# Optimization experiments

Hardware: AMD Instinct MI355X
Metric: run time of the kernel (lower is better)

Reference implementation:

```python
import jax, jax.numpy as jnp
import numpy as np

B, S, H = 8, 1024, 1024
NH, HD = 16, 64
MBANK, TOPK = 128, 16
NLAYERS, FF = 12, 4096
EPS = 1e-5


def _ln(x, w, b):
    m = x.mean(-1, keepdims=True)
    v = ((x - m) ** 2).mean(-1, keepdims=True)
    return (x - m) / jnp.sqrt(v + EPS) * w + b


def _split_heads(x):  # [B,S,H] -> [B,NH,S,HD]
    return x.reshape(B, S, NH, HD).transpose(0, 2, 1, 3)


def _sdpa(q, k, v):  # inputs [B,NH,S,HD]
    scores = jnp.einsum('bhqd,bhkd->bhqk', q, k) / jnp.sqrt(jnp.float32(HD))
    attn = jax.nn.softmax(scores, axis=-1)
    o = jnp.einsum('bhqk,bhkd->bhqd', attn, v)
    return o.transpose(0, 2, 1, 3).reshape(B, S, H)


def setup_inputs() -> dict:
    key = jax.random.key(0)
    ks = jax.random.split(key, 24)
    n = lambda k, shp, s=0.02: jax.random.normal(k, shp, jnp.float32) * s
    return {
        'hidden_states': jax.random.normal(ks[0], (B, S, H), jnp.float32),
        'ln1_w': jnp.ones((H,), jnp.float32), 'ln1_b': jnp.zeros((H,), jnp.float32),
        'ln2_w': jnp.ones((H,), jnp.float32), 'ln2_b': jnp.zeros((H,), jnp.float32),
        'rec_wq': n(ks[1], (H, H)), 'rec_wk': n(ks[2], (H, H)),
        'rec_wv': n(ks[3], (H, H)), 'rec_wo': n(ks[4], (H, H)),
        'rec_ad_w1': n(ks[5], (H // 4, H)), 'rec_ad_w2': n(ks[6], (H, H // 4)),
        'mem_bank': n(ks[7], (MBANK, H)),
        'alloc_w': n(ks[8], (MBANK, H)), 'alloc_b': jnp.zeros((MBANK,), jnp.float32),
        'retr_w': n(ks[9], (MBANK, H)), 'retr_b': jnp.zeros((MBANK,), jnp.float32),
        'upd_w': n(ks[10], (H, H)), 'upd_b': jnp.zeros((H,), jnp.float32),
        'mem_scales': jnp.full((NLAYERS,), 0.1, jnp.float32),
        'attn_in_w': n(ks[11], (3 * H, H)), 'attn_in_b': jnp.zeros((3 * H,), jnp.float32),
        'attn_out_w': n(ks[12], (H, H)), 'attn_out_b': jnp.zeros((H,), jnp.float32),
        'mlp_w1': n(ks[13], (FF, H)), 'mlp_b1': jnp.zeros((FF,), jnp.float32),
        'mlp_w2': n(ks[14], (H, FF)), 'mlp_b2': jnp.zeros((H,), jnp.float32),
        'layer_idx': 4,
    }


def reference(hidden_states, ln1_w, ln1_b, ln2_w, ln2_b,
              rec_wq, rec_wk, rec_wv, rec_wo, rec_ad_w1, rec_ad_w2,
              mem_bank, alloc_w, alloc_b, retr_w, retr_b, upd_w, upd_b, mem_scales,
              attn_in_w, attn_in_b, attn_out_w, attn_out_b,
              mlp_w1, mlp_b1, mlp_w2, mlp_b2, layer_idx):
    residual = hidden_states
    h = _ln(hidden_states, ln1_w, ln1_b)

    # --- CrossLayerParameterRecycler (layer_idx % 4 == 0 and > 0 -> recycle) ---
    if layer_idx % 4 == 0 and layer_idx > 0:
        q = _split_heads(h @ rec_wq.T)
        k = _split_heads(h @ rec_wk.T)
        v = _split_heads(h @ rec_wv.T)
        base_out = _sdpa(q, k, v) @ rec_wo.T
        h = jax.nn.relu(base_out @ rec_ad_w1.T) @ rec_ad_w2.T

    # --- CrossLayerMemoryManager ---
    pooled = h.mean(axis=1)                                  # [B,H]
    alloc_weights = jax.nn.softmax(pooled @ alloc_w.T + alloc_b, axis=-1)   # [B,MBANK]
    retr_weights = jax.nn.softmax(pooled @ retr_w.T + retr_b, axis=-1)
    retrieved = retr_weights @ mem_bank                      # [B,H]
    h = h + retrieved[:, None, :] * mem_scales[layer_idx]
    update_signals = jax.nn.sigmoid(h.mean(axis=1) @ upd_w.T + upd_b)       # [B,H]
    _, top_idx = jax.lax.top_k(alloc_weights, TOPK)          # [B,TOPK]

    # sequential per-batch scatter (later batches overwrite earlier, as in torch loop)
    def _write(mb, be):
        idx, sig = be
        return mb.at[idx].set(jnp.broadcast_to(sig, (TOPK, H))), None
    new_mem_bank, _ = jax.lax.scan(_write, mem_bank, (top_idx, update_signals))

    # --- self attention (nn.MultiheadAttention, batch_first) ---
    qkv = h @ attn_in_w.T + attn_in_b                        # [B,S,3H]
    q, k, v = jnp.split(qkv, 3, axis=-1)
    attn_out = _sdpa(_split_heads(q), _split_heads(k), _split_heads(v))
    attn_out = attn_out @ attn_out_w.T + attn_out_b
    h = residual + attn_out

    # --- MLP block ---
    residual2 = h
    h = _ln(h, ln2_w, ln2_b)
    h = jax.nn.gelu(h @ mlp_w1.T + mlp_b1, approximate=False) @ mlp_w2.T + mlp_b2
    out = residual2 + h
    return out, new_mem_bank
```

## Files before the change

kernel.cpp:

```cpp
#include <hip/hip_runtime.h>
#include <hip/hip_bf16.h>
#include <math.h>
#include <stdint.h>


#define BB 8
#define SS 1024
#define HH 1024
#define NHEAD 16
#define HD 64
#define MBANK 128
#define TOPK_N 16
#define FF_DIM 4096
#define MROWS (BB * SS)
#define NB_ELEM (8ull*1024*1024)

typedef __bf16 bf16x8 __attribute__((ext_vector_type(8)));
typedef __bf16 bf16x4 __attribute__((ext_vector_type(4)));
typedef float f32x4 __attribute__((ext_vector_type(4)));

#define SCALE_LOG2E 0.18033688011112042f

__device__ __forceinline__ unsigned short f2b(float x) {
  unsigned u = __float_as_uint(x);
  unsigned r = (u + 0x7FFFu + ((u >> 16) & 1u)) >> 16;
  return (unsigned short)r;
}
__device__ __forceinline__ float b2f(unsigned short u) {
  return __uint_as_float((unsigned)u << 16);
}

__device__ __forceinline__ float hmax4(f32x4 v) {
  return fmaxf(fmaxf(v[0], v[1]), fmaxf(v[2], v[3]));
}

__device__ __forceinline__ void load16_lds(const void* g, void* lds_base, int lane) {
#if __has_builtin(__builtin_amdgcn_global_load_lds)
  typedef const __attribute__((address_space(1))) unsigned int guint;
  typedef __attribute__((address_space(3))) unsigned int luint;
  __builtin_amdgcn_global_load_lds((guint*)(uintptr_t)g,
                                   (luint*)(unsigned long long)(unsigned int)(uintptr_t)lds_base,
                                   16, 0, 0);
#else
  *(uint4*)((char*)lds_base + lane * 16) = *(const uint4*)g;
#endif
}

__device__ __forceinline__ float gelu_exact(float x) {
  return 0.5f * x * (1.f + erff(x * 0.70710678118654752440f));
}


__global__ __launch_bounds__(256) void cast_split(const float* __restrict__ s,
                                                  unsigned short* __restrict__ hi,
                                                  unsigned short* __restrict__ lo, int n4) {
  int i = blockIdx.x * 256 + threadIdx.x;
  if (i < n4) {
    float4 v = ((const float4*)s)[i];
    ushort4 h, l;
    h.x = f2b(v.x); l.x = f2b(v.x - b2f(h.x));
    h.y = f2b(v.y); l.y = f2b(v.y - b2f(h.y));
    h.z = f2b(v.z); l.z = f2b(v.z - b2f(h.z));
    h.w = f2b(v.w); l.w = f2b(v.w - b2f(h.w));
    ((ushort4*)hi)[i] = h;
    ((ushort4*)lo)[i] = l;
  }
}

__global__ __launch_bounds__(256) void ln3(const float* __restrict__ x,
                                           const float* __restrict__ w,
                                           const float* __restrict__ b,
                                           unsigned short* __restrict__ yh,
                                           unsigned short* __restrict__ yl) {
  int row = blockIdx.x;
  const float* xr = x + (size_t)row * HH;
  int t = threadIdx.x;
  float v[4];
  float s = 0.f, ss = 0.f;
#pragma unroll
  for (int i = 0; i < 4; i++) {
    v[i] = xr[t + i * 256];
    s += v[i];
    ss += v[i] * v[i];
  }
  __shared__ float rs[8], rss[8];
  for (int o = 32; o > 0; o >>= 1) {
    s += __shfl_down(s, o, 64);
    ss += __shfl_down(ss, o, 64);
  }
  int wid = t >> 6, lane = t & 63;
  if (lane == 0) { rs[wid] = s; rss[wid] = ss; }
  __syncthreads();
  if (t == 0) {
    float S = rs[0] + rs[1] + rs[2] + rs[3];
    float SSum = rss[0] + rss[1] + rss[2] + rss[3];
    float m = S * (1.f / HH);
    float var = SSum * (1.f / HH) - m * m;
    rs[4] = m;
    rs[5] = rsqrtf(var + 1e-5f);
  }
  __syncthreads();
  float m = rs[4], inv = rs[5];
#pragma unroll
  for (int i = 0; i < 4; i++) {
    int c = t + i * 256;
    float y = (v[i] - m) * inv * w[c] + b[c];
    unsigned short h = f2b(y);
    yh[(size_t)row * HH + c] = h;
    yl[(size_t)row * HH + c] = f2b(y - b2f(h));
  }
}

template <int ACT, int MODE>
__global__ __launch_bounds__(256) void gemm3(const unsigned short* __restrict__ Ah,
                                             const unsigned short* __restrict__ Al, int lda,
                                             const unsigned short* __restrict__ Wh,
                                             const unsigned short* __restrict__ Wl, int ldw,
                                             unsigned short* __restrict__ Oh,
                                             unsigned short* __restrict__ Ol,
                                             float* __restrict__ outF,
                                             int ldo, int K) {
  __shared__ unsigned short Ash[128 * 32];
  __shared__ unsigned short Asl[128 * 32];
  __shared__ unsigned short Bsh[128 * 32];
  __shared__ unsigned short Bsl[128 * 32];
  int n0 = blockIdx.x * 128, m0 = blockIdx.y * 128;
  int t = threadIdx.x, w = t >> 6, L = t & 63, quad = L >> 4, l16 = L & 15;
  int wm = w & 1, wn = w >> 1;
  const f32x4 vzero = {0.f, 0.f, 0.f, 0.f};
  f32x4 acc[4][4];
#pragma unroll
  for (int i = 0; i < 4; i++)
#pragma unroll
    for (int j = 0; j < 4; j++) acc[i][j] = vzero;
  int srow = L >> 2;
  int scol = ((L & 3) ^ ((L >> 3) & 3)) * 8;
  int rsw = (l16 >> 1) & 3;
  for (int k0 = 0; k0 < K; k0 += 32) {
    __syncthreads();
#pragma unroll
    for (int c = 0; c < 2; c++) {
      int r = (c * 4 + w) * 16 + srow;
      size_t aoff = (size_t)(m0 + r) * lda + k0 + scol;
      size_t boff = (size_t)(n0 + r) * ldw + k0 + scol;
      load16_lds(Ah + aoff, &Ash[(c * 4 + w) * 512], L);
      load16_lds(Al + aoff, &Asl[(c * 4 + w) * 512], L);
      load16_lds(Wh + boff, &Bsh[(c * 4 + w) * 512], L);
      load16_lds(Wl + boff, &Bsl[(c * 4 + w) * 512], L);
    }
    __syncthreads();
    bf16x8 afh[4], afl[4], bfh[4], bfl[4];
#pragma unroll
    for (int i = 0; i < 4; i++) {
      int off = (wm * 64 + i * 16 + l16) * 32 + (quad ^ rsw) * 8;
      afh[i] = *(const bf16x8*)&Ash[off];
      afl[i] = *(const bf16x8*)&Asl[off];
    }
#pragma unroll
    for (int j = 0; j < 4; j++) {
      int off = (wn * 64 + j * 16 + l16) * 32 + (quad ^ rsw) * 8;
      bfh[j] = *(const bf16x8*)&Bsh[off];
      bfl[j] = *(const bf16x8*)&Bsl[off];
    }
#pragma unroll
    for (int i = 0; i < 4; i++)
#pragma unroll
      for (int j = 0; j < 4; j++) {
        acc[i][j] = __builtin_amdgcn_mfma_f32_16x16x32_bf16(afh[i], bfh[j], acc[i][j], 0, 0, 0);
        acc[i][j] = __builtin_amdgcn_mfma_f32_16x16x32_bf16(afh[i], bfl[j], acc[i][j], 0, 0, 0);
        acc[i][j] = __builtin_amdgcn_mfma_f32_16x16x32_bf16(afl[i], bfh[j], acc[i][j], 0, 0, 0);
      }
  }
#pragma unroll
  for (int i = 0; i < 4; i++) {
    int mb = m0 + wm * 64 + i * 16 + quad * 4;
#pragma unroll
    for (int j = 0; j < 4; j++) {
      int n = n0 + wn * 64 + j * 16 + l16;
      if (MODE == 1) {
        ushort4 sh, sl;
        float vv[4];
#pragma unroll
        for (int r = 0; r < 4; r++) {
          float v = acc[i][j][r];
          if (ACT == 1) v = fmaxf(v, 0.f);
          vv[r] = v;
        }
        sh.x = f2b(vv[0]); sl.x = f2b(vv[0] - b2f(sh.x));
        sh.y = f2b(vv[1]); sl.y = f2b(vv[1] - b2f(sh.y));
        sh.z = f2b(vv[2]); sl.z = f2b(vv[2] - b2f(sh.z));
        sh.w = f2b(vv[3]); sl.w = f2b(vv[3] - b2f(sh.w));
        *(ushort4*)&Oh[(size_t)n * ldo + mb] = sh;
        *(ushort4*)&Ol[(size_t)n * ldo + mb] = sl;
      } else {
#pragma unroll
        for (int r = 0; r < 4; r++) {
          float v = acc[i][j][r];
          if (ACT == 1) v = fmaxf(v, 0.f);
          size_t off = (size_t)(mb + r) * ldo + n;
          if (MODE == 0) {
            unsigned short h = f2b(v);
            Oh[off] = h;
            Ol[off] = f2b(v - b2f(h));
          } else {
            outF[off] = v;
          }
        }
      }
    }
  }
}

__global__ __launch_bounds__(256) void sdpa3(const unsigned short* __restrict__ Qh,
                                             const unsigned short* __restrict__ Ql,
                                             const unsigned short* __restrict__ Kh,
                                             const unsigned short* __restrict__ Kl,
                                             const unsigned short* __restrict__ Vth,
                                             const unsigned short* __restrict__ Vtl,
                                             unsigned short* __restrict__ Oh,
                                             unsigned short* __restrict__ Ol) {
  __shared__ unsigned short Ksh[64 * 64];
  __shared__ unsigned short Ksl[64 * 64];
  __shared__ unsigned short Vsh[64 * 64];
  __shared__ unsigned short Vsl[64 * 64];
  int qt = blockIdx.x, h = blockIdx.y, b = blockIdx.z;
  int t = threadIdx.x, w = t >> 6, L = t & 63, quad = L >> 4, l16 = L & 15;
  int q0 = qt * 64;
  const f32x4 vzero = {0.f, 0.f, 0.f, 0.f};
  bf16x8 qfh[2], qfl[2];
  {
    size_t qrow = (size_t)(b * SS + q0 + w * 16 + l16);
#pragma unroll
    for (int kh = 0; kh < 2; kh++) {
      size_t off = qrow * HH + h * 64 + kh * 32 + quad * 8;
      qfh[kh] = *(const bf16x8*)&Qh[off];
      qfl[kh] = *(const bf16x8*)&Ql[off];
    }
  }
  float mprev = -1e30f, lsum = 0.f;
  f32x4 oacc[4];
#pragma unroll
  for (int jd = 0; jd < 4; jd++) oacc[jd] = vzero;
  int srow = L >> 3;
  int scolV = ((L & 7) ^ srow) * 8;
  int rbase = ((l16 & 12) << 1) | (l16 & 3);
  int keyK = (l16 & 3) | (((l16 >> 2) & 1) << 2);
  int k7 = l16 & 7;
  for (int k0 = 0; k0 < SS; k0 += 64) {
    __syncthreads();
#pragma unroll
    for (int c = 0; c < 2; c++) {
      int rr = (c * 4 + w) * 8 + srow;
      int scolK = ((L & 7) ^ ((srow & 3) | (((c * 4 + w) & 1) << 2))) * 8;
      size_t koff = (size_t)(b * SS + k0 + rr) * HH + h * 64 + scolK;
      size_t voff = (size_t)(h * 64 + rr) * MROWS + b * SS + k0 + scolV;
      load16_lds(Kh + koff, &Ksh[(c * 4 + w) * 512], L);
      load16_lds(Kl + koff, &Ksl[(c * 4 + w) * 512], L);
      load16_lds(Vth + voff, &Vsh[(c * 4 + w) * 512], L);
      load16_lds(Vtl + voff, &Vsl[(c * 4 + w) * 512], L);
    }
    __syncthreads();
    f32x4 sacc[4];
#pragma unroll
    for (int jn = 0; jn < 4; jn++) sacc[jn] = vzero;
#pragma unroll
    for (int jn = 0; jn < 4; jn++) {
      int rowp = rbase + (jn & 1) * 4 + (jn >> 1) * 32;
#pragma unroll
      for (int kh = 0; kh < 2; kh++) {
        int off = rowp * 64 + (((kh * 4 + quad) ^ keyK) << 3);
        bf16x8 kfh = *(const bf16x8*)&Ksh[off];
        bf16x8 kfl = *(const bf16x8*)&Ksl[off];
        sacc[jn] = __builtin_amdgcn_mfma_f32_16x16x32_bf16(kfh, qfh[kh], sacc[jn], 0, 0, 0);
        sacc[jn] = __builtin_amdgcn_mfma_f32_16x16x32_bf16(kfl, qfh[kh], sacc[jn], 0, 0, 0);
        sacc[jn] = __builtin_amdgcn_mfma_f32_16x16x32_bf16(kfh, qfl[kh], sacc[jn], 0, 0, 0);
      }
    }
    float mt = fmaxf(fmaxf(hmax4(sacc[0]), hmax4(sacc[1])),
                     fmaxf(hmax4(sacc[2]), hmax4(sacc[3])));
    mt = fmaxf(mt, __shfl_xor(mt, 16, 64));
    mt = fmaxf(mt, __shfl_xor(mt, 32, 64));
    float m2 = fmaxf(mprev, mt * SCALE_LOG2E);
    float alpha = exp2f(mprev - m2);
    mprev = m2;
    float rs = 0.f;
    bf16x8 pah[2], pal[2];
#pragma unroll
    for (int jn = 0; jn < 4; jn++) {
      int kh = jn >> 1, half = (jn & 1) * 4;
#pragma unroll
      for (int r = 0; r < 4; r++) {
        float p = exp2f(fmaf(sacc[jn][r], SCALE_LOG2E, -m2));
        rs += p;
        __bf16 ph = (__bf16)p;
        pah[kh][half + r] = ph;
        pal[kh][half + r] = (__bf16)(p - (float)ph);
      }
    }
    rs += __shfl_xor(rs, 16, 64);
    rs += __shfl_xor(rs, 32, 64);
    lsum = lsum * alpha + rs;
    float ar[4];
#pragma unroll
    for (int r = 0; r < 4; r++) ar[r] = __shfl(alpha, quad * 4 + r, 16);
#pragma unroll
    for (int jd = 0; jd < 4; jd++)
#pragma unroll
      for (int r = 0; r < 4; r++) oacc[jd][r] *= ar[r];
#pragma unroll
    for (int jd = 0; jd < 4; jd++)
#pragma unroll
      for (int kh = 0; kh < 2; kh++) {
        int off = (jd * 16 + l16) * 64 + ((kh * 4 + quad) ^ k7) * 8;
        bf16x8 vfh = *(const bf16x8*)&Vsh[off];
        bf16x8 vfl = *(const bf16x8*)&Vsl[off];
        oacc[jd] = __builtin_amdgcn_mfma_f32_16x16x32_bf16(pah[kh], vfh, oacc[jd], 0, 0, 0);
        oacc[jd] = __builtin_amdgcn_mfma_f32_16x16x32_bf16(pah[kh], vfl, oacc[jd], 0, 0, 0);
        oacc[jd] = __builtin_amdgcn_mfma_f32_16x16x32_bf16(pal[kh], vfh, oacc[jd], 0, 0, 0);
      }
  }
  float inv = 1.f / lsum;
  float invr[4];
#pragma unroll
  for (int r = 0; r < 4; r++) invr[r] = __shfl(inv, quad * 4 + r, 16);
#pragma unroll
  for (int r = 0; r < 4; r++) {
    size_t row = (size_t)(b * SS + q0 + w * 16 + quad * 4 + r);
#pragma unroll
    for (int jd = 0; jd < 4; jd++) {
      float v = oacc[jd][r] * invr[r];
      unsigned short hh = f2b(v);
      size_t off = row * HH + h * 64 + jd * 16 + l16;
      Oh[off] = hh;
      Ol[off] = f2b(v - b2f(hh));
    }
  }
}


__global__ __launch_bounds__(256) void meanpool_kernel(const float* __restrict__ Hb,
                                                       float* __restrict__ P) {
  int cb = blockIdx.x;
  int b = blockIdx.y;
  int t = threadIdx.x;
  int c = (t & 63) + cb * 64;
  int part = t >> 6;
  float s = 0.f;
  const float* p = Hb + ((size_t)b * SS + part * 256) * HH + c;
  for (int j = 0; j < 256; j++) s += p[(size_t)j * HH];
  __shared__ float red[4][64];
  red[part][t & 63] = s;
  __syncthreads();
  if (t < 64) {
    float tot = red[0][t] + red[1][t] + red[2][t] + red[3][t];
    P[b * HH + cb * 64 + t] = tot * (1.f / SS);
  }
}

__global__ __launch_bounds__(256) void memlogits_kernel(const float* __restrict__ P,
                                                        const float* __restrict__ AW,
                                                        const float* __restrict__ ABias,
                                                        const float* __restrict__ RW,
                                                        const float* __restrict__ RBias,
                                                        float* __restrict__ LA,
                                                        float* __restrict__ LR) {
  int m = blockIdx.x, b = blockIdx.y;
  int t = threadIdx.x;
  const float* pr = P + b * HH;
  const float* aw = AW + (size_t)m * HH;
  const float* rw = RW + (size_t)m * HH;
  float sa = 0.f, sr = 0.f;
  for (int i = t; i < HH; i += 256) {
    float pv = pr[i];
    sa = fmaf(pv, aw[i], sa);
    sr = fmaf(pv, rw[i], sr);
  }
  for (int o = 32; o > 0; o >>= 1) {
    sa += __shfl_down(sa, o, 64);
    sr += __shfl_down(sr, o, 64);
  }
  __shared__ float ra[4], rr[4];
  if ((t & 63) == 0) { ra[t >> 6] = sa; rr[t >> 6] = sr; }
  __syncthreads();
  if (t == 0) {
    LA[b * MBANK + m] = ra[0] + ra[1] + ra[2] + ra[3] + ABias[m];
    LR[b * MBANK + m] = rr[0] + rr[1] + rr[2] + rr[3] + RBias[m];
  }
}

__global__ __launch_bounds__(256) void retrieve_kernel(const float* __restrict__ LA,
                                                       const float* __restrict__ LR,
                                                       const float* __restrict__ MB,
                                                       float* __restrict__ RET,
                                                       int* __restrict__ ISTOP) {
  int b = blockIdx.x;
  int t = threadIdx.x;
  __shared__ float rw[MBANK];
  __shared__ float la[MBANK];
  if (t < MBANK) {
    la[t] = LA[b * MBANK + t];
    rw[t] = LR[b * MBANK + t];
  }
  __syncthreads();
  if (t == 0) {
    float mx = -1e30f;
    for (int i = 0; i < MBANK; i++) mx = fmaxf(mx, rw[i]);
    float s = 0.f;
    for (int i = 0; i < MBANK; i++) {
      float e = __expf(rw[i] - mx);
      rw[i] = e;
      s += e;
    }
    float inv = 1.f / s;
    for (int i = 0; i < MBANK; i++) rw[i] *= inv;
  }
  __syncthreads();
  if (t < MBANK) {
    float mine = la[t];
    int rank = 0;
    for (int i = 0; i < MBANK; i++) {
      float o = la[i];
      if (o > mine || (o == mine && i < t)) rank++;
    }
    ISTOP[b * MBANK + t] = (rank < TOPK_N) ? 1 : 0;
  }
  for (int c = t; c < HH; c += 256) {
    float s = 0.f;
    for (int m = 0; m < MBANK; m++) s = fmaf(rw[m], MB[(size_t)m * HH + c], s);
    RET[b * HH + c] = s;
  }
}

__global__ __launch_bounds__(256) void addmem_kernel(float* __restrict__ Hb,
                                                     const float* __restrict__ RET,
                                                     const float* __restrict__ scales,
                                                     const int* __restrict__ lidx) {
  float sc = scales[lidx[0]];
  size_t i = (size_t)blockIdx.x * 256 + threadIdx.x;
  int c = (int)(i & 1023);
  int b = (int)(i >> 20);
  Hb[i] = fmaf(RET[b * HH + c], sc, Hb[i]);
}

__global__ __launch_bounds__(256) void upd_kernel(const float* __restrict__ P2,
                                                  const float* __restrict__ UW,
                                                  const float* __restrict__ UB,
                                                  float* __restrict__ UPD) {
  int n = blockIdx.x, b = blockIdx.y;
  int t = threadIdx.x;
  const float* pr = P2 + b * HH;
  const float* wr = UW + (size_t)n * HH;
  float s = 0.f;
  for (int i = t; i < HH; i += 256) s = fmaf(pr[i], wr[i], s);
  for (int o = 32; o > 0; o >>= 1) s += __shfl_down(s, o, 64);
  __shared__ float red[4];
  if ((t & 63) == 0) red[t >> 6] = s;
  __syncthreads();
  if (t == 0) {
    float tot = red[0] + red[1] + red[2] + red[3] + UB[n];
    UPD[b * HH + n] = 1.f / (1.f + __expf(-tot));
  }
}

__global__ __launch_bounds__(256) void membank_kernel(const float* __restrict__ MB,
                                                      const int* __restrict__ ISTOP,
                                                      const float* __restrict__ UPD,
                                                      float* __restrict__ OUT) {
  int row = blockIdx.x;
  int col = blockIdx.y * 256 + threadIdx.x;
  int w = -1;
  for (int b = 0; b < BB; b++)
    if (ISTOP[b * MBANK + row]) w = b;
  float v = (w >= 0) ? UPD[w * HH + col] : MB[(size_t)row * HH + col];
  OUT[(size_t)row * HH + col] = v;
}


__global__ __launch_bounds__(256) void ln_bf(const float* __restrict__ x,
                                             const float* __restrict__ w,
                                             const float* __restrict__ b,
                                             unsigned short* __restrict__ y) {
  int row = blockIdx.x;
  const float* xr = x + (size_t)row * HH;
  unsigned short* yr = y + (size_t)row * HH;
  int t = threadIdx.x;
  float v[4];
  float s = 0.f, ss = 0.f;
#pragma unroll
  for (int i = 0; i < 4; i++) {
    v[i] = xr[t + i * 256];
    s += v[i];
    ss += v[i] * v[i];
  }
  __shared__ float rs[8], rss[8];
  for (int o = 32; o > 0; o >>= 1) {
    s += __shfl_down(s, o, 64);
    ss += __shfl_down(ss, o, 64);
  }
  int wid = t >> 6, lane = t & 63;
  if (lane == 0) { rs[wid] = s; rss[wid] = ss; }
  __syncthreads();
  if (t == 0) {
    float S = rs[0] + rs[1] + rs[2] + rs[3];
    float SSum = rss[0] + rss[1] + rss[2] + rss[3];
    float m = S * (1.f / HH);
    float var = SSum * (1.f / HH) - m * m;
    rs[4] = m;
    rs[5] = rsqrtf(var + 1e-5f);
  }
  __syncthreads();
  float m = rs[4], inv = rs[5];
#pragma unroll
  for (int i = 0; i < 4; i++) {
    int c = t + i * 256;
    yr[c] = f2b((v[i] - m) * inv * w[c] + b[c]);
  }
}

__global__ __launch_bounds__(256) void castf2b(const float* __restrict__ s,
                                               unsigned short* __restrict__ d, int n4) {
  int i = blockIdx.x * 256 + threadIdx.x;
  if (i < n4) {
    float4 v = ((const float4*)s)[i];
    ushort4 o;
    o.x = f2b(v.x); o.y = f2b(v.y); o.z = f2b(v.z); o.w = f2b(v.w);
    ((ushort4*)d)[i] = o;
  }
}

template <int ACT, int MODE>
__global__ __launch_bounds__(256) void gemm_bf(const unsigned short* __restrict__ A, int lda,
                                               const unsigned short* __restrict__ W, int ldw,
                                               const float* __restrict__ bias,
                                               const float* __restrict__ resid,
                                               float* __restrict__ outF,
                                               unsigned short* __restrict__ outB,
                                               int ldo, int K) {
  __shared__ unsigned short As[128 * 32];
  __shared__ unsigned short Bs[128 * 32];
  int n0 = blockIdx.x * 128, m0 = blockIdx.y * 128;
  int t = threadIdx.x, w = t >> 6, L = t & 63, quad = L >> 4, l16 = L & 15;
  int wm = w & 1, wn = w >> 1;
  const f32x4 vzero = {0.f, 0.f, 0.f, 0.f};
  f32x4 acc[4][4];
#pragma unroll
  for (int i = 0; i < 4; i++)
#pragma unroll
    for (int j = 0; j < 4; j++) acc[i][j] = vzero;
  int srow = L >> 2;
  int scol = ((L & 3) ^ ((L >> 3) & 3)) * 8;
  int rsw = (l16 >> 1) & 3;
  for (int k0 = 0; k0 < K; k0 += 32) {
    __syncthreads();
#pragma unroll
    for (int c = 0; c < 2; c++) {
      int r = (c * 4 + w) * 16 + srow;
      load16_lds(A + (size_t)(m0 + r) * lda + k0 + scol, &As[(c * 4 + w) * 512], L);
      load16_lds(W + (size_t)(n0 + r) * ldw + k0 + scol, &Bs[(c * 4 + w) * 512], L);
    }
    __syncthreads();
    bf16x8 af[4], bfr[4];
#pragma unroll
    for (int i = 0; i < 4; i++)
      af[i] = *(const bf16x8*)&As[(wm * 64 + i * 16 + l16) * 32 + (quad ^ rsw) * 8];
#pragma unroll
    for (int j = 0; j < 4; j++)
      bfr[j] = *(const bf16x8*)&Bs[(wn * 64 + j * 16 + l16) * 32 + (quad ^ rsw) * 8];
#pragma unroll
    for (int i = 0; i < 4; i++)
#pragma unroll
      for (int j = 0; j < 4; j++)
        acc[i][j] = __builtin_amdgcn_mfma_f32_16x16x32_bf16(af[i], bfr[j], acc[i][j], 0, 0, 0);
  }
#pragma unroll
  for (int i = 0; i < 4; i++) {
    int mb = m0 + wm * 64 + i * 16 + quad * 4;
#pragma unroll
    for (int j = 0; j < 4; j++) {
      int n = n0 + wn * 64 + j * 16 + l16;
      float bv = bias ? bias[n] : 0.f;
      if (MODE == 2) {
        ushort4 st;
        float v0 = acc[i][j][0] + bv, v1 = acc[i][j][1] + bv;
        float v2 = acc[i][j][2] + bv, v3 = acc[i][j][3] + bv;
        if (ACT == 1) { v0 = fmaxf(v0, 0.f); v1 = fmaxf(v1, 0.f); v2 = fmaxf(v2, 0.f); v3 = fmaxf(v3, 0.f); }
        if (ACT == 2) { v0 = gelu_exact(v0); v1 = gelu_exact(v1); v2 = gelu_exact(v2); v3 = gelu_exact(v3); }
        st.x = f2b(v0); st.y = f2b(v1); st.z = f2b(v2); st.w = f2b(v3);
        *(ushort4*)&outB[(size_t)n * ldo + mb] = st;
      } else {
#pragma unroll
        for (int r = 0; r < 4; r++) {
          float v = acc[i][j][r] + bv;
          if (ACT == 1) v = fmaxf(v, 0.f);
          if (ACT == 2) v = gelu_exact(v);
          size_t off = (size_t)(mb + r) * ldo + n;
          if (MODE == 1) outB[off] = f2b(v);
          else if (MODE == 3) outF[off] += v;
          else if (MODE == 4) outF[off] = v + resid[off];
        }
      }
    }
  }
}

__global__ __launch_bounds__(256) void sdpa_bf(const unsigned short* __restrict__ Q,
                                               const unsigned short* __restrict__ Kb,
                                               const unsigned short* __restrict__ Vt,
                                               unsigned short* __restrict__ O) {
  __shared__ unsigned short Ks[64 * 64];
  __shared__ unsigned short Vs[64 * 64];
  int qt = blockIdx.x, h = blockIdx.y, b = blockIdx.z;
  int t = threadIdx.x, w = t >> 6, L = t & 63, quad = L >> 4, l16 = L & 15;
  int q0 = qt * 64;
  const f32x4 vzero = {0.f, 0.f, 0.f, 0.f};
  bf16x8 qf[2];
  {
    size_t qrow = (size_t)(b * SS + q0 + w * 16 + l16);
#pragma unroll
    for (int kh = 0; kh < 2; kh++)
      qf[kh] = *(const bf16x8*)&Q[qrow * HH + h * 64 + kh * 32 + quad * 8];
  }
  float mprev = -1e30f, lsum = 0.f;
  f32x4 oacc[4];
#pragma unroll
  for (int jd = 0; jd < 4; jd++) oacc[jd] = vzero;
  int srow = L >> 3;
  int scolV = ((L & 7) ^ srow) * 8;
  int rbase = ((l16 & 12) << 1) | (l16 & 3);
  int keyK = (l16 & 3) | (((l16 >> 2) & 1) << 2);
  int k7 = l16 & 7;
  for (int k0 = 0; k0 < SS; k0 += 64) {
    __syncthreads();
#pragma unroll
    for (int c = 0; c < 2; c++) {
      int rr = (c * 4 + w) * 8 + srow;
      int scolK = ((L & 7) ^ ((srow & 3) | (((c * 4 + w) & 1) << 2))) * 8;
      load16_lds(Kb + (size_t)(b * SS + k0 + rr) * HH + h * 64 + scolK, &Ks[(c * 4 + w) * 512], L);
      load16_lds(Vt + (size_t)(h * 64 + rr) * MROWS + b * SS + k0 + scolV, &Vs[(c * 4 + w) * 512], L);
    }
    __syncthreads();
    f32x4 sacc[4];
#pragma unroll
    for (int jn = 0; jn < 4; jn++) sacc[jn] = vzero;
#pragma unroll
    for (int jn = 0; jn < 4; jn++) {
      int rowp = rbase + (jn & 1) * 4 + (jn >> 1) * 32;
#pragma unroll
      for (int kh = 0; kh < 2; kh++) {
        bf16x8 kf = *(const bf16x8*)&Ks[rowp * 64 + (((kh * 4 + quad) ^ keyK) << 3)];
        sacc[jn] = __builtin_amdgcn_mfma_f32_16x16x32_bf16(kf, qf[kh], sacc[jn], 0, 0, 0);
      }
    }
    float mt = fmaxf(fmaxf(hmax4(sacc[0]), hmax4(sacc[1])),
                     fmaxf(hmax4(sacc[2]), hmax4(sacc[3])));
    mt = fmaxf(mt, __shfl_xor(mt, 16, 64));
    mt = fmaxf(mt, __shfl_xor(mt, 32, 64));
    float m2 = fmaxf(mprev, mt * SCALE_LOG2E);
    float alpha = exp2f(mprev - m2);
    mprev = m2;
    float rs = 0.f;
    bf16x8 pa[2];
#pragma unroll
    for (int jn = 0; jn < 4; jn++) {
      int kh = jn >> 1, half = (jn & 1) * 4;
#pragma unroll
      for (int r = 0; r < 4; r++) {
        float p = exp2f(fmaf(sacc[jn][r], SCALE_LOG2E, -m2));
        rs += p;
        pa[kh][half + r] = (__bf16)p;
      }
    }
    rs += __shfl_xor(rs, 16, 64);
    rs += __shfl_xor(rs, 32, 64);
    lsum = lsum * alpha + rs;
    float ar[4];
#pragma unroll
    for (int r = 0; r < 4; r++) ar[r] = __shfl(alpha, quad * 4 + r, 16);
#pragma unroll
    for (int jd = 0; jd < 4; jd++)
#pragma unroll
      for (int r = 0; r < 4; r++) oacc[jd][r] *= ar[r];
#pragma unroll
    for (int jd = 0; jd < 4; jd++)
#pragma unroll
      for (int kh = 0; kh < 2; kh++) {
        bf16x8 vf = *(const bf16x8*)&Vs[(jd * 16 + l16) * 64 + ((kh * 4 + quad) ^ k7) * 8];
        oacc[jd] = __builtin_amdgcn_mfma_f32_16x16x32_bf16(pa[kh], vf, oacc[jd], 0, 0, 0);
      }
  }
  float inv = 1.f / lsum;
  float invr[4];
#pragma unroll
  for (int r = 0; r < 4; r++) invr[r] = __shfl(inv, quad * 4 + r, 16);
#pragma unroll
  for (int r = 0; r < 4; r++) {
    size_t row = (size_t)(b * SS + q0 + w * 16 + quad * 4 + r);
#pragma unroll
    for (int jd = 0; jd < 4; jd++)
      O[row * HH + h * 64 + jd * 16 + l16] = f2b(oacc[jd][r] * invr[r]);
  }
}

extern "C" void kernel_launch(void* const* d_in, const int* in_sizes, int n_in,
                              void* d_out, int out_size, void* d_ws, size_t ws_size,
                              hipStream_t stream) {
  const float* x = (const float*)d_in[0];
  const float* ln1_w = (const float*)d_in[1];
  const float* ln1_b = (const float*)d_in[2];
  const float* ln2_w = (const float*)d_in[3];
  const float* ln2_b = (const float*)d_in[4];
  const float* rec_wq = (const float*)d_in[5];
  const float* rec_wk = (const float*)d_in[6];
  const float* rec_wv = (const float*)d_in[7];
  const float* rec_wo = (const float*)d_in[8];
  const float* rec_ad_w1 = (const float*)d_in[9];
  const float* rec_ad_w2 = (const float*)d_in[10];
  const float* mem_bank = (const float*)d_in[11];
  const float* alloc_w = (const float*)d_in[12];
  const float* alloc_b = (const float*)d_in[13];
  const float* retr_w = (const float*)d_in[14];
  const float* retr_b = (const float*)d_in[15];
  const float* upd_w = (const float*)d_in[16];
  const float* upd_b = (const float*)d_in[17];
  const float* mem_scales = (const float*)d_in[18];
  const float* attn_in_w = (const float*)d_in[19];
  const float* attn_in_b = (const float*)d_in[20];
  const float* attn_out_w = (const float*)d_in[21];
  const float* attn_out_b = (const float*)d_in[22];
  const float* mlp_w1 = (const float*)d_in[23];
  const float* mlp_b1 = (const float*)d_in[24];
  const float* mlp_w2 = (const float*)d_in[25];
  const float* mlp_b2 = (const float*)d_in[26];
  const int* layer_idx = (const int*)d_in[27];

  float* out = (float*)d_out;
  float* out_mb = out + NB_ELEM;

  const size_t U = NB_ELEM;
  unsigned short* W16 = (unsigned short*)d_ws;
  unsigned short* U0 = W16;
  unsigned short* U1 = W16 + U;
  unsigned short* U2 = W16 + 2 * U;
  unsigned short* U3 = W16 + 3 * U;
  unsigned short* U4 = W16 + 4 * U;
  unsigned short* U5 = W16 + 5 * U;
  unsigned short* wsh = W16 + 6 * U;
  unsigned short* wsl = wsh + 1048576;
  float* small = (float*)(wsl + 1048576);
  float* pooled = small;
  float* pooled2 = small + 8192;
  float* logitsA = small + 16384;
  float* logitsR = small + 17408;
  float* retrieved = small + 18432;
  float* updsig = small + 26624;
  int* istop = (int*)(small + 34816);
  unsigned short* D0 = (unsigned short*)out;
  unsigned short* D1 = D0 + U;
  unsigned short* ain_bf = U5;
  unsigned short* aout_bf = U5 + 3 * 1048576;

  dim3 blk(256);
  dim3 gG(8, 64);
  dim3 gG256(2, 64);
  dim3 gS(16, NHEAD, BB);
  const int EW_GRID = (int)(NB_ELEM / 256);

  ln3<<<MROWS, blk, 0, stream>>>(x, ln1_w, ln1_b, U0, U1);
  cast_split<<<1024, blk, 0, stream>>>(rec_wq, wsh, wsl, 262144);
  gemm3<0, 0><<<gG, blk, 0, stream>>>(U0, U1, HH, wsh, wsl, HH, U2, U3, nullptr, HH, HH);
  cast_split<<<1024, blk, 0, stream>>>(rec_wk, wsh, wsl, 262144);
  gemm3<0, 0><<<gG, blk, 0, stream>>>(U0, U1, HH, wsh, wsl, HH, U4, U5, nullptr, HH, HH);
  cast_split<<<1024, blk, 0, stream>>>(rec_wv, wsh, wsl, 262144);
  gemm3<0, 1><<<gG, blk, 0, stream>>>(U0, U1, HH, wsh, wsl, HH, D0, D1, nullptr, MROWS, HH);
  sdpa3<<<gS, blk, 0, stream>>>(U2, U3, U4, U5, D0, D1, U0, U1);
  cast_split<<<1024, blk, 0, stream>>>(rec_wo, wsh, wsl, 262144);
  gemm3<0, 0><<<gG, blk, 0, stream>>>(U0, U1, HH, wsh, wsl, HH, U2, U3, nullptr, HH, HH);
  cast_split<<<256, blk, 0, stream>>>(rec_ad_w1, wsh, wsl, 65536);
  gemm3<1, 0><<<gG256, blk, 0, stream>>>(U2, U3, HH, wsh, wsl, HH, U4, U4 + 2097152, nullptr, 256, HH);
  cast_split<<<256, blk, 0, stream>>>(rec_ad_w2, wsh, wsl, 65536);
  gemm3<0, 2><<<gG, blk, 0, stream>>>(U4, U4 + 2097152, 256, wsh, wsl, 256, nullptr, nullptr, out, HH, 256);
  meanpool_kernel<<<dim3(HH / 64, BB), blk, 0, stream>>>(out, pooled);
  memlogits_kernel<<<dim3(MBANK, BB), blk, 0, stream>>>(pooled, alloc_w, alloc_b, retr_w, retr_b, logitsA, logitsR);
  retrieve_kernel<<<BB, blk, 0, stream>>>(logitsA, logitsR, mem_bank, retrieved, istop);
  addmem_kernel<<<EW_GRID, blk, 0, stream>>>(out, retrieved, mem_scales, layer_idx);
  meanpool_kernel<<<dim3(HH / 64, BB), blk, 0, stream>>>(out, pooled2);
  upd_kernel<<<dim3(HH, BB), blk, 0, stream>>>(pooled2, upd_w, upd_b, updsig);
  membank_kernel<<<dim3(MBANK, HH / 256), blk, 0, stream>>>(mem_bank, istop, updsig, out_mb);
  castf2b<<<8192, blk, 0, stream>>>(out, U0, 2097152);
  castf2b<<<3072, blk, 0, stream>>>(attn_in_w, ain_bf, 786432);
  castf2b<<<1024, blk, 0, stream>>>(attn_out_w, aout_bf, 262144);
  gemm_bf<0, 1><<<gG, blk, 0, stream>>>(U0, HH, ain_bf, HH, attn_in_b, nullptr, nullptr, U1, HH, HH);
  gemm_bf<0, 1><<<gG, blk, 0, stream>>>(U0, HH, ain_bf + (size_t)HH * HH, HH, attn_in_b + HH, nullptr, nullptr, U2, HH, HH);
  gemm_bf<0, 2><<<gG, blk, 0, stream>>>(U0, HH, ain_bf + 2ull * HH * HH, HH, attn_in_b + 2 * HH, nullptr, nullptr, U3, MROWS, HH);
  sdpa_bf<<<gS, blk, 0, stream>>>(U1, U2, U3, U4);
  gemm_bf<0, 4><<<gG, blk, 0, stream>>>(U4, HH, aout_bf, HH, attn_out_b, x, out, nullptr, HH, HH);
  ln_bf<<<MROWS, blk, 0, stream>>>(out, ln2_w, ln2_b, U1);
  {
    unsigned short* w1b = U0;
    unsigned short* w2b = U0 + 4 * 1048576;
    unsigned short* h2 = U2;
    castf2b<<<4096, blk, 0, stream>>>(mlp_w1, w1b, 1048576);
    castf2b<<<4096, blk, 0, stream>>>(mlp_w2, w2b, 1048576);
    gemm_bf<2, 1><<<dim3(32, 64), blk, 0, stream>>>(U1, HH, w1b, HH, mlp_b1, nullptr, nullptr, h2, FF_DIM, HH);
    gemm_bf<0, 3><<<gG, blk, 0, stream>>>(h2, FF_DIM, w2b, FF_DIM, mlp_b2, nullptr, out, nullptr, HH, FF_DIM);
  }
}
```

Baseline: 1.254 ms.

## Double-buffer LDS tiles in both GEMM kernels to overlap loads with MFMA

Both GEMM kernels (the split-bf16 gemm3 and the plain gemm_bf) now use two LDS buffers. The next K-slice is staged asynchronously while the current one is consumed by MFMAs, which cuts the barrier count per slice from two to one and hides global-to-LDS latency. This doubles LDS use, to 64KB per block for gemm3, which may reduce occupancy. The loop assumes K is a multiple of 64.

```diff
diff --git a/kernel.cpp b/kernel.cpp
--- a/kernel.cpp
+++ b/kernel.cpp
@@ -120,10 +120,10 @@
                                              unsigned short* __restrict__ Ol,
                                              float* __restrict__ outF,
                                              int ldo, int K) {
-  __shared__ unsigned short Ash[128 * 32];
-  __shared__ unsigned short Asl[128 * 32];
-  __shared__ unsigned short Bsh[128 * 32];
-  __shared__ unsigned short Bsl[128 * 32];
+  __shared__ unsigned short Ash[2][128 * 32];
+  __shared__ unsigned short Asl[2][128 * 32];
+  __shared__ unsigned short Bsh[2][128 * 32];
+  __shared__ unsigned short Bsl[2][128 * 32];
   int n0 = blockIdx.x * 128, m0 = blockIdx.y * 128;
   int t = threadIdx.x, w = t >> 6, L = t & 63, quad = L >> 4, l16 = L & 15;
   int wm = w & 1, wn = w >> 1;
@@ -136,31 +136,32 @@
   int srow = L >> 2;
   int scol = ((L & 3) ^ ((L >> 3) & 3)) * 8;
   int rsw = (l16 >> 1) & 3;
-  for (int k0 = 0; k0 < K; k0 += 32) {
-    __syncthreads();
+
+  auto stage = [&](int buf, int k0) {
 #pragma unroll
     for (int c = 0; c < 2; c++) {
       int r = (c * 4 + w) * 16 + srow;
       size_t aoff = (size_t)(m0 + r) * lda + k0 + scol;
       size_t boff = (size_t)(n0 + r) * ldw + k0 + scol;
-      load16_lds(Ah + aoff, &Ash[(c * 4 + w) * 512], L);
-      load16_lds(Al + aoff, &Asl[(c * 4 + w) * 512], L);
-      load16_lds(Wh + boff, &Bsh[(c * 4 + w) * 512], L);
-      load16_lds(Wl + boff, &Bsl[(c * 4 + w) * 512], L);
-    }
-    __syncthreads();
+      load16_lds(Ah + aoff, &Ash[buf][(c * 4 + w) * 512], L);
+      load16_lds(Al + aoff, &Asl[buf][(c * 4 + w) * 512], L);
+      load16_lds(Wh + boff, &Bsh[buf][(c * 4 + w) * 512], L);
+      load16_lds(Wl + boff, &Bsl[buf][(c * 4 + w) * 512], L);
+    }
+  };
+  auto compute = [&](int buf) {
     bf16x8 afh[4], afl[4], bfh[4], bfl[4];
 #pragma unroll
     for (int i = 0; i < 4; i++) {
       int off = (wm * 64 + i * 16 + l16) * 32 + (quad ^ rsw) * 8;
-      afh[i] = *(const bf16x8*)&Ash[off];
-      afl[i] = *(const bf16x8*)&Asl[off];
+      afh[i] = *(const bf16x8*)&Ash[buf][off];
+      afl[i] = *(const bf16x8*)&Asl[buf][off];
     }
 #pragma unroll
     for (int j = 0; j < 4; j++) {
       int off = (wn * 64 + j * 16 + l16) * 32 + (quad ^ rsw) * 8;
-      bfh[j] = *(const bf16x8*)&Bsh[off];
-      bfl[j] = *(const bf16x8*)&Bsl[off];
+      bfh[j] = *(const bf16x8*)&Bsh[buf][off];
+      bfl[j] = *(const bf16x8*)&Bsl[buf][off];
     }
 #pragma unroll
     for (int i = 0; i < 4; i++)
@@ -170,6 +171,17 @@
         acc[i][j] = __builtin_amdgcn_mfma_f32_16x16x32_bf16(afh[i], bfl[j], acc[i][j], 0, 0, 0);
         acc[i][j] = __builtin_amdgcn_mfma_f32_16x16x32_bf16(afl[i], bfh[j], acc[i][j], 0, 0, 0);
       }
+  };
+
+  stage(0, 0);
+  __syncthreads();
+  for (int k0 = 0; k0 < K; k0 += 64) {
+    stage(1, k0 + 32);
+    compute(0);
+    __syncthreads();
+    if (k0 + 64 < K) stage(0, k0 + 64);
+    compute(1);
+    __syncthreads();
   }
 #pragma unroll
   for (int i = 0; i < 4; i++) {
@@ -536,8 +548,8 @@
                                                float* __restrict__ outF,
                                                unsigned short* __restrict__ outB,
                                                int ldo, int K) {
-  __shared__ unsigned short As[128 * 32];
-  __shared__ unsigned short Bs[128 * 32];
+  __shared__ unsigned short As[2][128 * 32];
+  __shared__ unsigned short Bs[2][128 * 32];
   int n0 = blockIdx.x * 128, m0 = blockIdx.y * 128;
   int t = threadIdx.x, w = t >> 6, L = t & 63, quad = L >> 4, l16 = L & 15;
   int wm = w & 1, wn = w >> 1;
@@ -550,27 +562,39 @@
   int srow = L >> 2;
   int scol = ((L & 3) ^ ((L >> 3) & 3)) * 8;
   int rsw = (l16 >> 1) & 3;
-  for (int k0 = 0; k0 < K; k0 += 32) {
-    __syncthreads();
+
+  auto stage = [&](int buf, int k0) {
 #pragma unroll
     for (int c = 0; c < 2; c++) {
       int r = (c * 4 + w) * 16 + srow;
-      load16_lds(A + (size_t)(m0 + r) * lda + k0 + scol, &As[(c * 4 + w) * 512], L);
-      load16_lds(W + (size_t)(n0 + r) * ldw + k0 + scol, &Bs[(c * 4 + w) * 512], L);
-    }
-    __syncthreads();
+      load16_lds(A + (size_t)(m0 + r) * lda + k0 + scol, &As[buf][(c * 4 + w) * 512], L);
+      load16_lds(W + (size_t)(n0 + r) * ldw + k0 + scol, &Bs[buf][(c * 4 + w) * 512], L);
+    }
+  };
+  auto compute = [&](int buf) {
     bf16x8 af[4], bfr[4];
 #pragma unroll
     for (int i = 0; i < 4; i++)
-      af[i] = *(const bf16x8*)&As[(wm * 64 + i * 16 + l16) * 32 + (quad ^ rsw) * 8];
+      af[i] = *(const bf16x8*)&As[buf][(wm * 64 + i * 16 + l16) * 32 + (quad ^ rsw) * 8];
 #pragma unroll
     for (int j = 0; j < 4; j++)
-      bfr[j] = *(const bf16x8*)&Bs[(wn * 64 + j * 16 + l16) * 32 + (quad ^ rsw) * 8];
+      bfr[j] = *(const bf16x8*)&Bs[buf][(wn * 64 + j * 16 + l16) * 32 + (quad ^ rsw) * 8];
 #pragma unroll
     for (int i = 0; i < 4; i++)
 #pragma unroll
       for (int j = 0; j < 4; j++)
         acc[i][j] = __builtin_amdgcn_mfma_f32_16x16x32_bf16(af[i], bfr[j], acc[i][j], 0, 0, 0);
+  };
+
+  stage(0, 0);
+  __syncthreads();
+  for (int k0 = 0; k0 < K; k0 += 64) {
+    stage(1, k0 + 32);
+    compute(0);
+    __syncthreads();
+    if (k0 + 64 < K) stage(0, k0 + 64);
+    compute(1);
+    __syncthreads();
   }
 #pragma unroll
   for (int i = 0; i < 4; i++) {
```

After: 1.136 ms. 9.4% less time.
